# Kernel optimization log

Hardware: AMD Instinct MI355X
Metric: run time of the kernel (lower is better)

The kernel has to match this reference:

```python
import jax, jax.numpy as jnp
import numpy as np

C = 128  # in_channels

def setup_inputs() -> dict:
    key = jax.random.key(0)
    k1, k2, k3, k4 = jax.random.split(key, 4)
    b, c, h, w = 4, C, 64, 64
    feature0 = jax.random.normal(k1, (b, c, h, w), dtype=jnp.float32)
    flow = jax.random.normal(k2, (b, 2, h, w), dtype=jnp.float32)
    # Linear weights stored torch-style as [out, in]; xavier-uniform-like scale
    lim = float(np.sqrt(6.0 / (c + c)))
    Wq = jax.random.uniform(k3, (c, c), minval=-lim, maxval=lim, dtype=jnp.float32)
    Wk = jax.random.uniform(k4, (c, c), minval=-lim, maxval=lim, dtype=jnp.float32)
    bq = jnp.zeros((c,), dtype=jnp.float32)
    bk = jnp.zeros((c,), dtype=jnp.float32)
    return {"feature0": feature0, "flow": flow, "Wq": Wq, "bq": bq, "Wk": Wk, "bk": bk}

def reference(feature0, flow, Wq, bq, Wk, bk):
    b, c, h, w = feature0.shape
    n = h * w
    # [b, n, c]
    x = feature0.reshape(b, c, n).transpose(0, 2, 1)
    query = x @ Wq.T + bq                     # q_proj(feature0)
    key = query @ Wk.T + bk                   # NOTE: k_proj applied to query (as in source)
    value = flow.reshape(b, flow.shape[1], n).transpose(0, 2, 1)  # [b, n, 2]
    scores = jnp.einsum('bnc,bmc->bnm', query, key) / jnp.sqrt(jnp.float32(c))
    prob = jax.nn.softmax(scores, axis=-1)    # [b, n, n]
    out = jnp.einsum('bnm,bmv->bnv', prob, value)  # [b, n, 2]
    return out.reshape(b, h, w, value.shape[-1]).transpose(0, 3, 1, 2)
```

## Files before the change

### kernel.cpp

```cpp
#include <hip/hip_runtime.h>
#include <hip/hip_bf16.h>

constexpr int CH = 128;
constexpr int NPOS = 4096;
constexpr int NB = 4;
constexpr int SPLITS = 8;

typedef __bf16 bf16x8 __attribute__((ext_vector_type(8)));
typedef float f32x2 __attribute__((ext_vector_type(2)));
typedef float f32x16 __attribute__((ext_vector_type(16)));

constexpr float CSC = 0.08838834764831845f * 1.4426950408889634f;


__device__ __forceinline__ void async_copy16(const void* g, void* l) {
  auto gp = (const __attribute__((address_space(1))) unsigned int*)((uintptr_t)g);
  auto lp = (__attribute__((address_space(3))) unsigned int*)((uintptr_t)l);
  __builtin_amdgcn_global_load_lds(gp, lp, 16, 0, 0);
}

#define PIPE_BARRIER(N)                                              \
  asm volatile("s_waitcnt vmcnt(" #N ") lgkmcnt(0)\n\ts_barrier" ::: "memory")

__global__ __launch_bounds__(128) void fuse_w_kernel(
    const float* __restrict__ Wq, const float* __restrict__ bq,
    const float* __restrict__ Wk, const float* __restrict__ bk,
    __bf16* __restrict__ Wqb, __bf16* __restrict__ Wqkb,
    float* __restrict__ bqk) {
  __shared__ float red[CH];
  const int o = blockIdx.x;
  const int i = threadIdx.x;
  float acc = 0.f;
#pragma unroll 8
  for (int m = 0; m < CH; m++) acc += Wk[o * CH + m] * Wq[m * CH + i];
  Wqkb[o * CH + i] = (__bf16)acc;
  Wqb[o * CH + i] = (__bf16)Wq[o * CH + i];
  red[i] = Wk[o * CH + i] * bq[i];
  __syncthreads();
  if (i == 0) {
    float s = 0.f;
    for (int m = 0; m < CH; m++) s += red[m];
    bqk[o] = s + bk[o];
  }
}

__global__ __launch_bounds__(512) void proj_kernel(
    const float* __restrict__ feature0, const __bf16* __restrict__ Wqb,
    const float* __restrict__ bq, const __bf16* __restrict__ Wqkb,
    const float* __restrict__ bqk, __bf16* __restrict__ Qf,
    __bf16* __restrict__ Kf) {
  __shared__ __bf16 Alds[8 * 512];

  const int bid = blockIdx.x;
  const int b = (bid >> 1) & 3;
  const int u = (bid >> 3) * 2 + (bid & 1);
  const int tid = threadIdx.x;
  const int lane = tid & 63;
  const int half = lane >> 5, l31 = lane & 31;
  const int wv = tid >> 6;
  const int z = wv >> 2, n = wv & 3;

  {
    const int p = tid & 31;
    const int c0 = tid >> 5;
    const float* src = feature0 + (size_t)(b * CH) * NPOS + u * 32 + p;
#pragma unroll
    for (int r = 0; r < 8; r++) {
      const int c = r * 16 + c0;
      const float v = src[(size_t)c * NPOS];
      const int ks = c >> 4, hf = (c >> 3) & 1, j = c & 7;
      Alds[ks * 512 + (p + 32 * hf) * 8 + j] = (__bf16)v;
    }
  }
  __syncthreads();

  bf16x8 A[8];
#pragma unroll
  for (int ks = 0; ks < 8; ks++)
    A[ks] = *(const bf16x8*)(&Alds[ks * 512 + lane * 8]);

  const __bf16* W = z ? Wqkb : Wqb;
  const float* bias = z ? bqk : bq;
  __bf16* Out = z ? Kf : Qf;
  const float scale = z ? 1.0f : CSC;

  const int co = n * 32 + l31;
  const bf16x8* Bp = (const bf16x8*)(W + co * CH + half * 8);
  f32x16 c = {0.f, 0.f, 0.f, 0.f, 0.f, 0.f, 0.f, 0.f,
              0.f, 0.f, 0.f, 0.f, 0.f, 0.f, 0.f, 0.f};
#pragma unroll
  for (int ks = 0; ks < 8; ks++)
    c = __builtin_amdgcn_mfma_f32_32x32x16_bf16(A[ks], Bp[ks * 2], c, 0, 0, 0);
  const float bv = bias[co];
  const int kf = n * 2 + (l31 >> 4);
  const int lanebit = (l31 >> 3) & 1;
  const int j = l31 & 7;
#pragma unroll
  for (int r = 0; r < 16; r++) {
    int roff = (r & 3) + 8 * (r >> 2) + 4 * half;
    Out[((((size_t)(b * (NPOS / 32) + u)) * 8 + kf) * 64 +
         (roff + 32 * lanebit)) * 8 + j] = (__bf16)((c[r] + bv) * scale);
  }
}

__global__ __launch_bounds__(256, 2) void attn_kernel(
    const __bf16* __restrict__ Qf, const __bf16* __restrict__ Kf,
    const float* __restrict__ flow, float* __restrict__ part) {
  __shared__ __bf16 Klds[3][8 * 512];
  __shared__ float flds[2 * 512];
  __shared__ float red[256 * 3];

  const int bid = blockIdx.x;
  const int b = (bid >> 1) & 3;
  const int u = (bid >> 3) * 2 + (bid & 1);
  const int split = u >> 4;
  const int qg = u & 15;

  const int tid = threadIdx.x;
  const int wave = tid >> 6, lane = tid & 63;
  const int half = lane >> 5, l31 = lane & 31;
  const int kbase = split * (NPOS / SPLITS);
  constexpr int NT = NPOS / SPLITS / 32;

  {
    const float* fl0 = flow + (size_t)(b * 2 + 0) * NPOS + kbase;
    const float* fl1 = flow + (size_t)(b * 2 + 1) * NPOS + kbase;
    flds[tid] = fl0[tid];
    flds[256 + tid] = fl0[256 + tid];
    flds[512 + tid] = fl1[tid];
    flds[768 + tid] = fl1[256 + tid];
  }

  const int qt0 = qg * 8 + wave * 2;
  bf16x8 qf0[8], qf1[8];
  {
    const bf16x8* Qp =
        (const bf16x8*)Qf + ((size_t)(b * (NPOS / 32) + qt0) * 8) * 64 + lane;
#pragma unroll
    for (int kf = 0; kf < 8; kf++) {
      qf0[kf] = Qp[kf * 64];
      qf1[kf] = Qp[512 + kf * 64];
    }
  }

  const __bf16* Ktb = Kf + ((size_t)(b * (NPOS / 32) + (kbase >> 5))) * 4096;

  auto issue = [&](int t, int buf) {
    const __bf16* g = Ktb + (size_t)t * 4096;
    const int c0 = wave * 1024;
    async_copy16(g + c0 + lane * 8, &Klds[buf][c0 + lane * 8]);
    async_copy16(g + c0 + 512 + lane * 8, &Klds[buf][c0 + 512 + lane * 8]);
  };
  issue(0, 0);
  issue(1, 1);

  float ls0[16], ls1[16];
  f32x2 av0[16], av1[16];
#pragma unroll
  for (int r = 0; r < 16; r++) {
    ls0[r] = 0.f;
    ls1[r] = 0.f;
    av0[r] = f32x2{0.f, 0.f};
    av1[r] = f32x2{0.f, 0.f};
  }

  int bcur = 0, bnext = 2;
  for (int t = 0; t < NT; t++) {
    if (t < NT - 1) {
      PIPE_BARRIER(2);
    } else {
      PIPE_BARRIER(0);
    }
    if (t + 2 < NT) issue(t + 2, bnext);

    const __bf16* kb = &Klds[bcur][0];
    f32x16 c0 = {0.f, 0.f, 0.f, 0.f, 0.f, 0.f, 0.f, 0.f,
                 0.f, 0.f, 0.f, 0.f, 0.f, 0.f, 0.f, 0.f};
    f32x16 c1 = {0.f, 0.f, 0.f, 0.f, 0.f, 0.f, 0.f, 0.f,
                 0.f, 0.f, 0.f, 0.f, 0.f, 0.f, 0.f, 0.f};
#pragma unroll
    for (int kf = 0; kf < 8; kf++) {
      bf16x8 bfrag = *(const bf16x8*)(kb + kf * 512 + lane * 8);
      c0 = __builtin_amdgcn_mfma_f32_32x32x16_bf16(qf0[kf], bfrag, c0, 0, 0, 0);
      c1 = __builtin_amdgcn_mfma_f32_32x32x16_bf16(qf1[kf], bfrag, c1, 0, 0, 0);
    }
    const f32x2 v01 = {flds[t * 32 + l31], flds[512 + t * 32 + l31]};
#pragma unroll
    for (int r = 0; r < 16; r++) {
      float p0 = __builtin_amdgcn_exp2f(c0[r]);
      ls0[r] += p0;
      av0[r] += f32x2{p0, p0} * v01;
      float p1 = __builtin_amdgcn_exp2f(c1[r]);
      ls1[r] += p1;
      av1[r] += f32x2{p1, p1} * v01;
    }
    bcur = (bcur == 2) ? 0 : bcur + 1;
    bnext = (bnext == 2) ? 0 : bnext + 1;
  }

#pragma unroll
  for (int r = 0; r < 16; r++) {
#pragma unroll
    for (int st = 1; st < 32; st <<= 1) {
      ls0[r] += __shfl_xor(ls0[r], st, 64);
      av0[r][0] += __shfl_xor(av0[r][0], st, 64);
      av0[r][1] += __shfl_xor(av0[r][1], st, 64);
      ls1[r] += __shfl_xor(ls1[r], st, 64);
      av1[r][0] += __shfl_xor(av1[r][0], st, 64);
      av1[r][1] += __shfl_xor(av1[r][1], st, 64);
    }
  }
  if (l31 == 0) {
#pragma unroll
    for (int r = 0; r < 16; r++) {
      int roff = (r & 3) + 8 * (r >> 2) + 4 * half;
      int ql0 = (wave * 2 + 0) * 32 + roff;
      int ql1 = (wave * 2 + 1) * 32 + roff;
      red[ql0 * 3 + 0] = ls0[r];
      red[ql0 * 3 + 1] = av0[r][0];
      red[ql0 * 3 + 2] = av0[r][1];
      red[ql1 * 3 + 0] = ls1[r];
      red[ql1 * 3 + 1] = av1[r][0];
      red[ql1 * 3 + 2] = av1[r][1];
    }
  }
  __syncthreads();
  for (int idx = tid; idx < 256 * 3; idx += 256) {
    int plane = idx >> 8, ql = idx & 255;
    part[((size_t)(plane * SPLITS + split) * NB + b) * NPOS + qg * 256 + ql] =
        red[ql * 3 + plane];
  }
}

__global__ __launch_bounds__(256) void combine_kernel(
    const float* __restrict__ part, float* __restrict__ out) {
  int t = blockIdx.x * 256 + threadIdx.x;
  int b = t >> 12, q = t & (NPOS - 1);
  float l = 0.f, x = 0.f, y = 0.f;
#pragma unroll
  for (int s = 0; s < SPLITS; s++) {
    l += part[((size_t)(0 * SPLITS + s) * NB + b) * NPOS + q];
    x += part[((size_t)(1 * SPLITS + s) * NB + b) * NPOS + q];
    y += part[((size_t)(2 * SPLITS + s) * NB + b) * NPOS + q];
  }
  float inv = 1.0f / l;
  out[(size_t)(b * 2 + 0) * NPOS + q] = x * inv;
  out[(size_t)(b * 2 + 1) * NPOS + q] = y * inv;
}

extern "C" void kernel_launch(void* const* d_in, const int* in_sizes, int n_in,
                              void* d_out, int out_size, void* d_ws,
                              size_t ws_size, hipStream_t stream) {
  const float* feature0 = (const float*)d_in[0];
  const float* flow = (const float*)d_in[1];
  const float* Wq = (const float*)d_in[2];
  const float* bq = (const float*)d_in[3];
  const float* Wk = (const float*)d_in[4];
  const float* bk = (const float*)d_in[5];
  float* out = (float*)d_out;

  char* ws = (char*)d_ws;
  __bf16* Qf = (__bf16*)ws;
  __bf16* Kf = (__bf16*)(ws + (4 << 20));
  __bf16* Wqb = (__bf16*)(ws + (8 << 20));
  __bf16* Wqkb = (__bf16*)(ws + (8 << 20) + (32 << 10));
  float* bqk = (float*)(ws + (8 << 20) + (64 << 10));
  float* part = (float*)(ws + (8 << 20) + (128 << 10));

  fuse_w_kernel<<<dim3(CH), 128, 0, stream>>>(Wq, bq, Wk, bk, Wqb, Wqkb, bqk);
  proj_kernel<<<dim3(512), 512, 0, stream>>>(feature0, Wqb, bq, Wqkb, bqk, Qf,
                                             Kf);
  attn_kernel<<<dim3(512), 256, 0, stream>>>(Qf, Kf, flow, part);
  combine_kernel<<<dim3(NB * NPOS / 256), 256, 0, stream>>>(part, out);
}
```

Measured before the change: 113.8 us.

## Load K fragments directly from global and double the key splits

The attention kernel no longer stages K tiles into LDS through async global-to-LDS copies and a triple-buffered barrier pipeline. Each wave now reads its bf16x8 K fragments straight from global memory, relying on L2/L1 because all four waves share the same K tile. The key dimension is split 16 ways instead of 8, doubling the grid to 1024 blocks for more parallelism at the cost of more partial results for the combine step. The risk is exposed global-load latency with no explicit prefetch, and four waves redundantly fetching the same data.

Result: slower. 140.4 us (+23.4%).

```diff
diff --git a/kernel.cpp b/kernel.cpp
--- a/kernel.cpp
+++ b/kernel.cpp
@@ -4,7 +4,7 @@
 constexpr int CH = 128;
 constexpr int NPOS = 4096;
 constexpr int NB = 4;
-constexpr int SPLITS = 8;
+constexpr int SPLITS = 16;
 
 typedef __bf16 bf16x8 __attribute__((ext_vector_type(8)));
 typedef float f32x2 __attribute__((ext_vector_type(2)));
@@ -12,15 +12,6 @@
 
 constexpr float CSC = 0.08838834764831845f * 1.4426950408889634f;
 
-
-__device__ __forceinline__ void async_copy16(const void* g, void* l) {
-  auto gp = (const __attribute__((address_space(1))) unsigned int*)((uintptr_t)g);
-  auto lp = (__attribute__((address_space(3))) unsigned int*)((uintptr_t)l);
-  __builtin_amdgcn_global_load_lds(gp, lp, 16, 0, 0);
-}
-
-#define PIPE_BARRIER(N)                                              \
-  asm volatile("s_waitcnt vmcnt(" #N ") lgkmcnt(0)\n\ts_barrier" ::: "memory")
 
 __global__ __launch_bounds__(128) void fuse_w_kernel(
     const float* __restrict__ Wq, const float* __restrict__ bq,
@@ -106,8 +97,7 @@
 __global__ __launch_bounds__(256, 2) void attn_kernel(
     const __bf16* __restrict__ Qf, const __bf16* __restrict__ Kf,
     const float* __restrict__ flow, float* __restrict__ part) {
-  __shared__ __bf16 Klds[3][8 * 512];
-  __shared__ float flds[2 * 512];
+  __shared__ float flds[2 * (NPOS / SPLITS)];
   __shared__ float red[256 * 3];
 
   const int bid = blockIdx.x;
@@ -126,10 +116,9 @@
     const float* fl0 = flow + (size_t)(b * 2 + 0) * NPOS + kbase;
     const float* fl1 = flow + (size_t)(b * 2 + 1) * NPOS + kbase;
     flds[tid] = fl0[tid];
-    flds[256 + tid] = fl0[256 + tid];
-    flds[512 + tid] = fl1[tid];
-    flds[768 + tid] = fl1[256 + tid];
-  }
+    flds[256 + tid] = fl1[tid];
+  }
+  __syncthreads();
 
   const int qt0 = qg * 8 + wave * 2;
   bf16x8 qf0[8], qf1[8];
@@ -143,16 +132,9 @@
     }
   }
 
-  const __bf16* Ktb = Kf + ((size_t)(b * (NPOS / 32) + (kbase >> 5))) * 4096;
-
-  auto issue = [&](int t, int buf) {
-    const __bf16* g = Ktb + (size_t)t * 4096;
-    const int c0 = wave * 1024;
-    async_copy16(g + c0 + lane * 8, &Klds[buf][c0 + lane * 8]);
-    async_copy16(g + c0 + 512 + lane * 8, &Klds[buf][c0 + 512 + lane * 8]);
-  };
-  issue(0, 0);
-  issue(1, 1);
+  const bf16x8* Ktb =
+      (const bf16x8*)(Kf + ((size_t)(b * (NPOS / 32) + (kbase >> 5))) * 4096) +
+      lane;
 
   float ls0[16], ls1[16];
   f32x2 av0[16], av1[16];
@@ -164,27 +146,19 @@
     av1[r] = f32x2{0.f, 0.f};
   }
 
-  int bcur = 0, bnext = 2;
   for (int t = 0; t < NT; t++) {
-    if (t < NT - 1) {
-      PIPE_BARRIER(2);
-    } else {
-      PIPE_BARRIER(0);
-    }
-    if (t + 2 < NT) issue(t + 2, bnext);
-
-    const __bf16* kb = &Klds[bcur][0];
+    const bf16x8* kb = Ktb + (size_t)t * 512;
     f32x16 c0 = {0.f, 0.f, 0.f, 0.f, 0.f, 0.f, 0.f, 0.f,
                  0.f, 0.f, 0.f, 0.f, 0.f, 0.f, 0.f, 0.f};
     f32x16 c1 = {0.f, 0.f, 0.f, 0.f, 0.f, 0.f, 0.f, 0.f,
                  0.f, 0.f, 0.f, 0.f, 0.f, 0.f, 0.f, 0.f};
 #pragma unroll
     for (int kf = 0; kf < 8; kf++) {
-      bf16x8 bfrag = *(const bf16x8*)(kb + kf * 512 + lane * 8);
+      bf16x8 bfrag = kb[kf * 64];
       c0 = __builtin_amdgcn_mfma_f32_32x32x16_bf16(qf0[kf], bfrag, c0, 0, 0, 0);
       c1 = __builtin_amdgcn_mfma_f32_32x32x16_bf16(qf1[kf], bfrag, c1, 0, 0, 0);
     }
-    const f32x2 v01 = {flds[t * 32 + l31], flds[512 + t * 32 + l31]};
+    const f32x2 v01 = {flds[t * 32 + l31], flds[256 + t * 32 + l31]};
 #pragma unroll
     for (int r = 0; r < 16; r++) {
       float p0 = __builtin_amdgcn_exp2f(c0[r]);
@@ -194,8 +168,6 @@
       ls1[r] += p1;
       av1[r] += f32x2{p1, p1} * v01;
     }
-    bcur = (bcur == 2) ? 0 : bcur + 1;
-    bnext = (bnext == 2) ? 0 : bnext + 1;
   }
 
 #pragma unroll
@@ -270,6 +242,6 @@
   fuse_w_kernel<<<dim3(CH), 128, 0, stream>>>(Wq, bq, Wk, bk, Wqb, Wqkb, bqk);
   proj_kernel<<<dim3(512), 512, 0, stream>>>(feature0, Wqb, bq, Wqkb, bqk, Qf,
                                              Kf);
-  attn_kernel<<<dim3(512), 256, 0, stream>>>(Qf, Kf, flow, part);
+  attn_kernel<<<dim3(NB * SPLITS * 16), 256, 0, stream>>>(Qf, Kf, flow, part);
   combine_kernel<<<dim3(NB * NPOS / 256), 256, 0, stream>>>(part, out);
 }
```
